# Performance work log

Measured on AMD Instinct MI355X. Metric: run time of the kernel, lower is better.

Reference implementation:

```python
import jax, jax.numpy as jnp
import numpy as np

BN_EPS = 1e-5
LN_EPS = 1e-5

N_NODES = 50000
N_EDGES = 800000
D_IN = 128
D_HID = 512


def _batchnorm(h, gamma, beta):
    # training-mode BatchNorm1d: biased variance over the node/batch dim
    m = jnp.mean(h, axis=0)
    v = jnp.mean(jnp.square(h - m), axis=0)
    return (h - m) * jax.lax.rsqrt(v + BN_EPS) * gamma + beta


def setup_inputs() -> dict:
    key = jax.random.key(0)
    ks = jax.random.split(key, 8)
    x = jax.random.normal(ks[0], (N_NODES, D_IN), dtype=jnp.float32)
    edge_index = jax.random.randint(ks[1], (2, N_EDGES), 0, N_NODES, dtype=jnp.int64)
    s1 = 1.0 / np.sqrt(D_IN)
    s2 = 1.0 / np.sqrt(D_HID)
    W1 = jax.random.uniform(ks[2], (D_IN, D_HID), jnp.float32, -s1, s1)
    b1 = jax.random.uniform(ks[3], (D_HID,), jnp.float32, -s1, s1)
    W2 = jax.random.uniform(ks[4], (D_HID, D_IN), jnp.float32, -s2, s2)
    b2 = jax.random.uniform(ks[5], (D_IN,), jnp.float32, -s2, s2)
    return {
        "x": x,
        "edge_index": edge_index,
        "W1": W1, "b1": b1,
        "bn1_g": jnp.ones((D_HID,), jnp.float32), "bn1_b": jnp.zeros((D_HID,), jnp.float32),
        "W2": W2, "b2": b2,
        "bn2_g": jnp.ones((D_IN,), jnp.float32), "bn2_b": jnp.zeros((D_IN,), jnp.float32),
        "ln_g": jnp.ones((D_IN,), jnp.float32), "ln_b": jnp.zeros((D_IN,), jnp.float32),
    }


def reference(x, edge_index, W1, b1, bn1_g, bn1_b, W2, b2, bn2_g, bn2_b, ln_g, ln_b):
    n = x.shape[0]
    src = edge_index[0]
    dst = edge_index[1]
    # GIN aggregation: sum of neighbor (source) features at each destination node
    agg = jax.ops.segment_sum(x[src], dst, num_segments=n)  # [N, D_IN]
    h = x + agg  # (1 + eps) * x + agg, eps = 0
    # MLP: Linear -> BN -> ReLU -> Linear -> BN -> ReLU (final activation)
    h = jax.nn.relu(_batchnorm(h @ W1 + b1, bn1_g, bn1_b))  # [N, D_HID]
    h = jax.nn.relu(_batchnorm(h @ W2 + b2, bn2_g, bn2_b))  # [N, D_IN]
    # residual + LayerNorm (dropout p=0 -> identity)
    out = h + x
    m = jnp.mean(out, axis=-1, keepdims=True)
    v = jnp.mean(jnp.square(out - m), axis=-1, keepdims=True)
    out = (out - m) * jax.lax.rsqrt(v + LN_EPS) * ln_g + ln_b
    return out
```

## Files before the change

### kernel.cpp

```cpp
#include <hip/hip_runtime.h>
#include <stdint.h>

#define N_NODES 50000
#define N_EDGES 800000
#define D_IN    128
#define D_HID   512
#define NPAD    50048
#define SCAN_NB 196
#define G_TILES 782
#define G_BLOCKS 128

typedef __attribute__((ext_vector_type(8))) short short8;
typedef __attribute__((ext_vector_type(4))) float f32x4;

__device__ __forceinline__ float bf2f(unsigned short u) {
    union { unsigned int i; float f; } v; v.i = ((unsigned int)u) << 16; return v.f;
}
__device__ __forceinline__ unsigned short f2bf(float f) {
    union { float f; unsigned int i; } v; v.f = f;
    unsigned int r = v.i + 0x7fffu + ((v.i >> 16) & 1u);
    return (unsigned short)(r >> 16);
}
__device__ __forceinline__ float loadP(const void* p, long i, int isf) {
    return isf ? ((const float*)p)[i] : bf2f(((const unsigned short*)p)[i]);
}

__global__ void k_init(const void* __restrict__ x, const int* __restrict__ ei,
                       float* __restrict__ stats, int* __restrict__ counts,
                       int* __restrict__ flags) {
    int t = threadIdx.x;
    if (blockIdx.x < 197) {
        int i = blockIdx.x * 256 + t;
        if (i < 384) stats[1024 + i] = 0.f;
        else if (i < 384 + N_NODES) counts[i - 384] = 0;
    } else {
        __shared__ int sh[2];
        if (t == 0) { sh[0] = 0; sh[1] = 1; }
        __syncthreads();
        const unsigned short* xu = (const unsigned short*)x;
        for (int i = t; i < 8192; i += 256)
            if (((xu[i] >> 7) & 0xFF) == 0xFF) sh[0] = 1;
        for (int k = t; k < 64; k += 256)
            if (ei[2 * k + 1] != 0) sh[1] = 0;
        __syncthreads();
        if (t == 0) { flags[0] = sh[0]; flags[1] = sh[1]; }
    }
}

__global__ void k_transpose2(const void* __restrict__ W1, const void* __restrict__ W2,
                             unsigned short* __restrict__ w1t, unsigned short* __restrict__ w2t,
                             const int* __restrict__ flags) {
    int isf = flags[0];
    int idx = blockIdx.x * 256 + threadIdx.x;
    if (idx < D_IN * D_HID) {
        int n = idx >> 7, k = idx & 127;
        int src = k * D_HID + n;
        w1t[idx] = isf ? f2bf(((const float*)W1)[src])
                       : ((const unsigned short*)W1)[src];
    } else {
        int j = idx - D_IN * D_HID;
        int n = j >> 9, k = j & 511;
        int src = k * D_IN + n;
        w2t[j] = isf ? f2bf(((const float*)W2)[src])
                     : ((const unsigned short*)W2)[src];
    }
}

__global__ void k_count(const int* __restrict__ ei, int* __restrict__ counts,
                        const int* __restrict__ flags) {
    int i64 = flags[1];
    int e = blockIdx.x * 256 + threadIdx.x;
    int d = i64 ? ei[2 * N_EDGES + 2 * e] : ei[N_EDGES + e];
    d = min(max(d, 0), N_NODES - 1);
    atomicAdd(&counts[d], 1);
}

__global__ __launch_bounds__(256) void k_scan_block(const int* __restrict__ counts,
                                                    int* __restrict__ rowptr,
                                                    int* __restrict__ partials) {
    __shared__ int a[256], b[256];
    int t = threadIdx.x;
    int idx = blockIdx.x * 256 + t;
    int c = (idx < N_NODES) ? counts[idx] : 0;
    a[t] = c;
    __syncthreads();
    int* src = a; int* dst = b;
    for (int off = 1; off < 256; off <<= 1) {
        dst[t] = src[t] + ((t >= off) ? src[t - off] : 0);
        __syncthreads();
        int* tmp = src; src = dst; dst = tmp;
    }
    if (idx < N_NODES) rowptr[idx] = src[t] - c;
    if (t == 255) partials[blockIdx.x] = src[255];
}

__global__ __launch_bounds__(256) void k_scan_part(int* __restrict__ partials) {
    __shared__ int a[256], b[256];
    int t = threadIdx.x;
    int c = (t < SCAN_NB) ? partials[t] : 0;
    a[t] = c;
    __syncthreads();
    int* src = a; int* dst = b;
    for (int off = 1; off < 256; off <<= 1) {
        dst[t] = src[t] + ((t >= off) ? src[t - off] : 0);
        __syncthreads();
        int* tmp = src; src = dst; dst = tmp;
    }
    if (t < SCAN_NB) partials[t] = src[t] - c;
}

__global__ void k_scan_add(int* __restrict__ rowptr, int* __restrict__ cursor,
                           const int* __restrict__ partials) {
    int idx = blockIdx.x * 256 + threadIdx.x;
    if (idx < N_NODES) {
        int v = rowptr[idx] + partials[blockIdx.x];
        rowptr[idx] = v;
        cursor[idx] = v;
    } else if (idx == N_NODES) {
        rowptr[N_NODES] = N_EDGES;
    }
}

__global__ void k_fill(const int* __restrict__ ei, int* __restrict__ cursor,
                       int* __restrict__ bucket, const int* __restrict__ flags) {
    int i64 = flags[1];
    int e = blockIdx.x * 256 + threadIdx.x;
    int s, d;
    if (i64) { s = ei[2 * e]; d = ei[2 * N_EDGES + 2 * e]; }
    else     { s = ei[e];     d = ei[N_EDGES + e]; }
    s = min(max(s, 0), N_NODES - 1);
    d = min(max(d, 0), N_NODES - 1);
    int pos = atomicAdd(&cursor[d], 1);
    bucket[pos] = s;
}

__global__ __launch_bounds__(256) void k_gather(const int* __restrict__ rowptr,
                                                const int* __restrict__ bucket,
                                                const void* __restrict__ x,
                                                unsigned short* __restrict__ agg,
                                                const int* __restrict__ flags) {
    int isf = flags[0];
    int w = threadIdx.x >> 6, lane = threadIdx.x & 63;
    int row = blockIdx.x * 4 + w;
    float a0 = 0.f, a1 = 0.f;
    if (row < N_NODES) {
        int beg = rowptr[row], end = rowptr[row + 1];
        if (isf) {
            const float* xf = (const float*)x;
            float2 v = *(const float2*)(xf + (size_t)row * D_IN + lane * 2);
            a0 = v.x; a1 = v.y;
            int j = beg;
            for (; j + 4 <= end; j += 4) {
                int s0 = bucket[j], s1 = bucket[j + 1], s2 = bucket[j + 2], s3 = bucket[j + 3];
                float2 n0 = *(const float2*)(xf + (size_t)s0 * D_IN + lane * 2);
                float2 n1 = *(const float2*)(xf + (size_t)s1 * D_IN + lane * 2);
                float2 n2 = *(const float2*)(xf + (size_t)s2 * D_IN + lane * 2);
                float2 n3 = *(const float2*)(xf + (size_t)s3 * D_IN + lane * 2);
                a0 += (n0.x + n1.x) + (n2.x + n3.x);
                a1 += (n0.y + n1.y) + (n2.y + n3.y);
            }
            for (; j < end; j++) {
                float2 n = *(const float2*)(xf + (size_t)bucket[j] * D_IN + lane * 2);
                a0 += n.x; a1 += n.y;
            }
        } else {
            const unsigned int* xu = (const unsigned int*)x;
            unsigned int u = xu[(size_t)row * 64 + lane];
            a0 = bf2f(u & 0xffff); a1 = bf2f(u >> 16);
            int j = beg;
            for (; j + 4 <= end; j += 4) {
                int s0 = bucket[j], s1 = bucket[j + 1], s2 = bucket[j + 2], s3 = bucket[j + 3];
                unsigned int u0 = xu[(size_t)s0 * 64 + lane];
                unsigned int u1 = xu[(size_t)s1 * 64 + lane];
                unsigned int u2 = xu[(size_t)s2 * 64 + lane];
                unsigned int u3 = xu[(size_t)s3 * 64 + lane];
                a0 += (bf2f(u0 & 0xffff) + bf2f(u1 & 0xffff)) + (bf2f(u2 & 0xffff) + bf2f(u3 & 0xffff));
                a1 += (bf2f(u0 >> 16) + bf2f(u1 >> 16)) + (bf2f(u2 >> 16) + bf2f(u3 >> 16));
            }
            for (; j < end; j++) {
                unsigned int n = xu[(size_t)bucket[j] * 64 + lane];
                a0 += bf2f(n & 0xffff); a1 += bf2f(n >> 16);
            }
        }
    }
    unsigned int o = (unsigned int)f2bf(a0) | ((unsigned int)f2bf(a1) << 16);
    ((unsigned int*)agg)[(size_t)row * 64 + lane] = o;
}

__global__ __launch_bounds__(256) void k_gram(const unsigned short* __restrict__ aggb,
                                              float* __restrict__ Gpart,
                                              float* __restrict__ colsum) {
    __shared__ unsigned short ldsT[128 * 64];
    int t = threadIdx.x;
    int wid = t >> 6, lane = t & 63;
    int wm = wid & 1, wn = wid >> 1;
    int quad = lane >> 4, l16 = lane & 15;
    f32x4 acc[4][4] = {};
    float cs = 0.f;
    int cscol = t & 127, cskh = t >> 7;
    for (int tile = blockIdx.x; tile < G_TILES; tile += G_BLOCKS) {
        __syncthreads();
        size_t rowbase = (size_t)tile * 64;
#pragma unroll
        for (int jj = 0; jj < 2; jj++) {
            int j = t + jj * 256;
            int c = j >> 5, rp = j & 31;
            uint4 v0 = *(const uint4*)(aggb + (rowbase + 2 * rp) * 128 + c * 8);
            uint4 v1 = *(const uint4*)(aggb + (rowbase + 2 * rp + 1) * 128 + c * 8);
            const unsigned short* p0 = (const unsigned short*)&v0;
            const unsigned short* p1 = (const unsigned short*)&v1;
            int k = 2 * rp, kc = k >> 3, ko = k & 7;
#pragma unroll
            for (int e = 0; e < 8; e++) {
                int col = c * 8 + e;
                *(unsigned int*)(ldsT + col * 64 + ((kc ^ (col & 7)) * 8) + ko) =
                    (unsigned int)p0[e] | ((unsigned int)p1[e] << 16);
            }
        }
        __syncthreads();
#pragma unroll
        for (int ksub = 0; ksub < 2; ksub++) {
            short8 fa[4], fb[4];
#pragma unroll
            for (int mt = 0; mt < 4; mt++) {
                int col = wm * 64 + mt * 16 + l16;
                fa[mt] = *(const short8*)(ldsT + col * 64 + (((ksub * 4 + quad) ^ (col & 7)) * 8));
            }
#pragma unroll
            for (int nt = 0; nt < 4; nt++) {
                int col = wn * 64 + nt * 16 + l16;
                fb[nt] = *(const short8*)(ldsT + col * 64 + (((ksub * 4 + quad) ^ (col & 7)) * 8));
            }
#pragma unroll
            for (int mt = 0; mt < 4; mt++)
#pragma unroll
                for (int nt = 0; nt < 4; nt++)
                    acc[mt][nt] = __builtin_amdgcn_mfma_f32_16x16x32_bf16(fa[mt], fb[nt], acc[mt][nt], 0, 0, 0);
        }
#pragma unroll
        for (int kc = 0; kc < 4; kc++) {
            short8 v = *(const short8*)(ldsT + cscol * 64 + (((cskh * 4 + kc) ^ (cscol & 7)) * 8));
#pragma unroll
            for (int e = 0; e < 8; e++) cs += bf2f((unsigned short)v[e]);
        }
    }
    float* gp = Gpart + (size_t)blockIdx.x * 16384;
#pragma unroll
    for (int mt = 0; mt < 4; mt++)
#pragma unroll
        for (int nt = 0; nt < 4; nt++) {
            int m = wm * 64 + mt * 16 + quad * 4;
            int n = wn * 64 + nt * 16 + l16;
#pragma unroll
            for (int rg = 0; rg < 4; rg++)
                gp[(m + rg) * 128 + n] = acc[mt][nt][rg];
        }
    atomicAdd(&colsum[cscol], cs);
}

__global__ void k_gred(const float* __restrict__ Gpart, float* __restrict__ G) {
    int i = blockIdx.x * 256 + threadIdx.x;
    float s = 0.f;
#pragma unroll 8
    for (int b = 0; b < G_BLOCKS; b++) s += Gpart[(size_t)b * 16384 + i];
    G[i] = s;
}

__global__ __launch_bounds__(256) void k_bn1(const float* __restrict__ G,
                                             const float* __restrict__ colsum,
                                             const unsigned short* __restrict__ w1t,
                                             const void* __restrict__ b1,
                                             float* __restrict__ sum1,
                                             float* __restrict__ sumsq1,
                                             const int* __restrict__ flags) {
    int isf = flags[0];
    __shared__ float wsh[4][128];
    int t = threadIdx.x, wid = t >> 6, lane = t & 63;
    int n = blockIdx.x * 4 + wid;
    unsigned int u = *(const unsigned int*)(w1t + (size_t)n * 128 + lane * 2);
    wsh[wid][lane * 2] = bf2f(u & 0xffff);
    wsh[wid][lane * 2 + 1] = bf2f(u >> 16);
    __syncthreads();
    const float* w = wsh[wid];
    const f32x4* g0 = (const f32x4*)(G + (size_t)lane * 128);
    const f32x4* g1 = (const f32x4*)(G + (size_t)(lane + 64) * 128);
    float t0 = 0.f, t1 = 0.f;
#pragma unroll 4
    for (int q4 = 0; q4 < 32; q4++) {
        f32x4 a = g0[q4], b = g1[q4];
        float w0 = w[q4 * 4], w1 = w[q4 * 4 + 1], w2 = w[q4 * 4 + 2], w3 = w[q4 * 4 + 3];
        t0 += a[0] * w0 + a[1] * w1 + a[2] * w2 + a[3] * w3;
        t1 += b[0] * w0 + b[1] * w1 + b[2] * w2 + b[3] * w3;
    }
    float sq = w[lane] * t0 + w[lane + 64] * t1;
    float s  = w[lane] * colsum[lane] + w[lane + 64] * colsum[lane + 64];
#pragma unroll
    for (int m = 1; m < 64; m <<= 1) {
        sq += __shfl_xor(sq, m, 64);
        s  += __shfl_xor(s, m, 64);
    }
    if (lane == 0) {
        float b = loadP(b1, n, isf);
        sum1[n]   = s + (float)N_NODES * b;
        sumsq1[n] = sq + 2.f * b * s + (float)N_NODES * b * b;
    }
}

__global__ __launch_bounds__(256, 2) void k_fused(const unsigned short* aggb,
                                                  const unsigned short* __restrict__ w1t,
                                                  const unsigned short* __restrict__ w2t,
                                                  const void* __restrict__ b1,
                                                  const void* __restrict__ b2,
                                                  const void* __restrict__ g1,
                                                  const void* __restrict__ bb1,
                                                  const float* __restrict__ sum1,
                                                  const float* __restrict__ sumsq1,
                                                  unsigned short* h2,
                                                  float* __restrict__ sum2,
                                                  float* __restrict__ sumsq2,
                                                  const int* __restrict__ flags) {
    __shared__ unsigned short bufW[128 * 128];
    __shared__ unsigned short bufA[128 * 128];
    int isf = flags[0];
    int t = threadIdx.x;
    int m0 = blockIdx.x * 128;
    int r = t >> 1, half = t & 1;
    int wid = t >> 6, lane = t & 63;
    int wm = wid & 1, wn = wid >> 1;
    int quad = lane >> 4, l16 = lane & 15;
#pragma unroll
    for (int i = 0; i < 8; i++) {
        int chunk = half * 8 + i;
        *(uint4*)(bufA + r * 128 + ((chunk ^ (r & 15)) * 8)) =
            *(const uint4*)(aggb + (size_t)(m0 + r) * 128 + chunk * 8);
    }
    __syncthreads();
    short8 ax[4][4];
#pragma unroll
    for (int ks = 0; ks < 4; ks++)
#pragma unroll
        for (int mt = 0; mt < 4; mt++)
            ax[ks][mt] = *(const short8*)(bufA + (wm * 64 + mt * 16 + l16) * 128 + (((ks * 4 + quad) ^ l16) * 8));
    f32x4 acc2[4][4] = {};
    for (int nb = 0; nb < 4; nb++) {
        __syncthreads();
#pragma unroll
        for (int i = 0; i < 8; i++) {
            int chunk = half * 8 + i;
            *(uint4*)(bufW + r * 128 + ((chunk ^ (r & 15)) * 8)) =
                *(const uint4*)(w1t + (size_t)(nb * 128 + r) * 128 + chunk * 8);
        }
        __syncthreads();
        f32x4 acc1[4][4] = {};
#pragma unroll
        for (int ks = 0; ks < 4; ks++) {
            short8 bw[4];
#pragma unroll
            for (int nt = 0; nt < 4; nt++)
                bw[nt] = *(const short8*)(bufW + (wn * 64 + nt * 16 + l16) * 128 + (((ks * 4 + quad) ^ l16) * 8));
#pragma unroll
            for (int mt = 0; mt < 4; mt++)
#pragma unroll
                for (int nt = 0; nt < 4; nt++)
                    acc1[mt][nt] = __builtin_amdgcn_mfma_f32_16x16x32_bf16(ax[ks][mt], bw[nt], acc1[mt][nt], 0, 0, 0);
        }
#pragma unroll
        for (int nt = 0; nt < 4; nt++) {
            int nl = wn * 64 + nt * 16 + l16;
            int n1 = nb * 128 + nl;
            float mz = sum1[n1] * (1.f / N_NODES);
            float vz = sumsq1[n1] * (1.f / N_NODES) - mz * mz;
            float inv = rsqrtf(fmaxf(vz, 0.f) + 1e-5f);
            float A = loadP(g1, n1, isf) * inv;
            float C = loadP(bb1, n1, isf) - mz * A + loadP(b1, n1, isf) * A;
            int ccw = nl >> 3, cl = nl & 7;
#pragma unroll
            for (int mt = 0; mt < 4; mt++)
#pragma unroll
                for (int rg = 0; rg < 4; rg++) {
                    int R = wm * 64 + mt * 16 + quad * 4 + rg;
                    bufA[R * 128 + ((ccw ^ (R & 15)) * 8) + cl] = f2bf(fmaxf(acc1[mt][nt][rg] * A + C, 0.f));
                }
        }
        __syncthreads();
#pragma unroll
        for (int i = 0; i < 8; i++) {
            int chunk = half * 8 + i;
            *(uint4*)(bufW + r * 128 + ((chunk ^ (r & 15)) * 8)) =
                *(const uint4*)(w2t + (size_t)r * D_HID + nb * 128 + chunk * 8);
        }
        __syncthreads();
#pragma unroll
        for (int ks = 0; ks < 4; ks++) {
            short8 aa[4], bw[4];
#pragma unroll
            for (int mt = 0; mt < 4; mt++)
                aa[mt] = *(const short8*)(bufA + (wm * 64 + mt * 16 + l16) * 128 + (((ks * 4 + quad) ^ l16) * 8));
#pragma unroll
            for (int nt = 0; nt < 4; nt++)
                bw[nt] = *(const short8*)(bufW + (wn * 64 + nt * 16 + l16) * 128 + (((ks * 4 + quad) ^ l16) * 8));
#pragma unroll
            for (int mt = 0; mt < 4; mt++)
#pragma unroll
                for (int nt = 0; nt < 4; nt++)
                    acc2[mt][nt] = __builtin_amdgcn_mfma_f32_16x16x32_bf16(aa[mt], bw[nt], acc2[mt][nt], 0, 0, 0);
        }
    }
#pragma unroll
    for (int nt = 0; nt < 4; nt++) {
        int n = wn * 64 + nt * 16 + l16;
        float bias = loadP(b2, n, isf);
        float s = 0.f, ss = 0.f;
#pragma unroll
        for (int mt = 0; mt < 4; mt++) {
            int Rb = m0 + wm * 64 + mt * 16 + quad * 4;
#pragma unroll
            for (int rg = 0; rg < 4; rg++) {
                float z = acc2[mt][nt][rg] + bias;
                h2[(size_t)(Rb + rg) * D_IN + n] = f2bf(z);
                if (Rb + rg < N_NODES) { s += z; ss += z * z; }
            }
        }
        s += __shfl_xor(s, 16, 64); ss += __shfl_xor(ss, 16, 64);
        s += __shfl_xor(s, 32, 64); ss += __shfl_xor(ss, 32, 64);
        if (quad == 0) { atomicAdd(&sum2[n], s); atomicAdd(&sumsq2[n], ss); }
    }
}

__global__ __launch_bounds__(256) void k_final(const unsigned short* __restrict__ h2,
                                               const void* __restrict__ x,
                                               const float* __restrict__ sum2,
                                               const float* __restrict__ sumsq2,
                                               const void* __restrict__ g2,
                                               const void* __restrict__ bb2,
                                               const void* __restrict__ lng,
                                               const void* __restrict__ lnb,
                                               void* __restrict__ out,
                                               const int* __restrict__ flags) {
    int isf = flags[0];
    __shared__ float a2s[D_IN], c2s[D_IN];
    int t = threadIdx.x;
    if (t < D_IN) {
        float m = sum2[t] * (1.f / N_NODES);
        float v = sumsq2[t] * (1.f / N_NODES) - m * m;
        float inv = rsqrtf(fmaxf(v, 0.f) + 1e-5f);
        float a = loadP(g2, t, isf) * inv;
        a2s[t] = a;
        c2s[t] = loadP(bb2, t, isf) - m * a;
    }
    __syncthreads();
    int w = t >> 6, lane = t & 63;
    int row = blockIdx.x * 4 + w;
    if (row >= N_NODES) return;
    size_t base = (size_t)row * D_IN;
    int c0 = lane * 2, c1 = lane * 2 + 1;
    unsigned int hu = ((const unsigned int*)h2)[base / 2 + lane];
    float x0, x1;
    if (isf) {
        float2 xv = *((const float2*)x + base / 2 + lane);
        x0 = xv.x; x1 = xv.y;
    } else {
        unsigned int xu = ((const unsigned int*)x)[base / 2 + lane];
        x0 = bf2f(xu & 0xffff); x1 = bf2f(xu >> 16);
    }
    float o0 = fmaxf(a2s[c0] * bf2f(hu & 0xffff) + c2s[c0], 0.f) + x0;
    float o1 = fmaxf(a2s[c1] * bf2f(hu >> 16) + c2s[c1], 0.f) + x1;
    float s = o0 + o1, ss = o0 * o0 + o1 * o1;
#pragma unroll
    for (int m = 1; m < 64; m <<= 1) {
        s += __shfl_xor(s, m, 64);
        ss += __shfl_xor(ss, m, 64);
    }
    float mean = s * (1.f / D_IN);
    float var = ss * (1.f / D_IN) - mean * mean;
    float inv = rsqrtf(fmaxf(var, 0.f) + 1e-5f);
    float r0 = (o0 - mean) * inv * loadP(lng, c0, isf) + loadP(lnb, c0, isf);
    float r1 = (o1 - mean) * inv * loadP(lng, c1, isf) + loadP(lnb, c1, isf);
    if (isf) {
        *((float2*)out + base / 2 + lane) = make_float2(r0, r1);
    } else {
        ((unsigned int*)out)[base / 2 + lane] = (unsigned int)f2bf(r0) | ((unsigned int)f2bf(r1) << 16);
    }
}

extern "C" void kernel_launch(void* const* d_in, const int* in_sizes, int n_in,
                              void* d_out, int out_size, void* d_ws, size_t ws_size,
                              hipStream_t stream) {
    const void* x    = d_in[0];
    const int*  ei   = (const int*)d_in[1];
    const void* W1   = d_in[2];
    const void* b1   = d_in[3];
    const void* bn1g = d_in[4];
    const void* bn1b = d_in[5];
    const void* W2   = d_in[6];
    const void* b2   = d_in[7];
    const void* bn2g = d_in[8];
    const void* bn2b = d_in[9];
    const void* lng  = d_in[10];
    const void* lnb  = d_in[11];

    char* ws = (char*)d_ws;
    float* stats   = (float*)ws;
    float* sum1    = stats;
    float* sumsq1  = stats + 512;
    float* sum2    = stats + 1024;
    float* sumsq2  = stats + 1152;
    float* colsum  = stats + 1280;
    int*   flags   = (int*)(ws + 5632);
    int*   partials= (int*)(ws + 5696);
    int*   rowptr  = (int*)(ws + 8192);
    int*   cursor  = (int*)(ws + 208256);
    unsigned short* w1t = (unsigned short*)(ws + 408320);
    unsigned short* w2t = (unsigned short*)(ws + 539392);
    float* G       = (float*)(ws + 670464);
    float* Gpart   = (float*)(ws + 736000);
    int*   bucket  = (int*)(ws + 9124608);
    unsigned short* agg = (unsigned short*)(ws + 12324608);
    unsigned short* h2  = agg;

    k_init<<<198, 256, 0, stream>>>(x, ei, stats, cursor, flags);
    k_transpose2<<<512, 256, 0, stream>>>(W1, W2, w1t, w2t, flags);
    k_count<<<N_EDGES / 256, 256, 0, stream>>>(ei, cursor, flags);
    k_scan_block<<<SCAN_NB, 256, 0, stream>>>(cursor, rowptr, partials);
    k_scan_part<<<1, 256, 0, stream>>>(partials);
    k_scan_add<<<SCAN_NB, 256, 0, stream>>>(rowptr, cursor, partials);
    k_fill<<<N_EDGES / 256, 256, 0, stream>>>(ei, cursor, bucket, flags);
    k_gather<<<NPAD / 4, 256, 0, stream>>>(rowptr, bucket, x, agg, flags);
    k_gram<<<G_BLOCKS, 256, 0, stream>>>(agg, Gpart, colsum);
    k_gred<<<64, 256, 0, stream>>>(Gpart, G);
    k_bn1<<<128, 256, 0, stream>>>(G, colsum, w1t, b1, sum1, sumsq1, flags);
    k_fused<<<NPAD / 128, 256, 0, stream>>>(agg, w1t, w2t, b1, b2, bn1g, bn1b,
                                            sum1, sumsq1, h2, sum2, sumsq2, flags);
    k_final<<<(N_NODES + 3) / 4, 256, 0, stream>>>(h2, x, sum2, sumsq2, bn2g, bn2b, lng, lnb, d_out, flags);
}
```

Baseline: 398.8 us.

## Halve fused MLP row tile to 64 and stage h2 stores through LDS

Shrinks the k_fused row tile from 128 to 64 nodes per block. This halves the accumulator registers and the activation LDS buffer, raises launch bounds to 3 blocks per SM, and doubles the grid for better occupancy and load balance across CUs. The h2 output is now written into LDS first and then stored with coalesced 16-byte writes instead of scattered 2-byte stores. The trade-off is that each block reloads all W1/W2 weight tiles for only 64 rows, which doubles weight traffic, and the extra syncs add overhead.

```diff
diff --git a/kernel.cpp b/kernel.cpp
--- a/kernel.cpp
+++ b/kernel.cpp
@@ -306,7 +306,7 @@
     }
 }
 
-__global__ __launch_bounds__(256, 2) void k_fused(const unsigned short* aggb,
+__global__ __launch_bounds__(256, 3) void k_fused(const unsigned short* aggb,
                                                   const unsigned short* __restrict__ w1t,
                                                   const unsigned short* __restrict__ w2t,
                                                   const void* __restrict__ b1,
@@ -320,38 +320,41 @@
                                                   float* __restrict__ sumsq2,
                                                   const int* __restrict__ flags) {
     __shared__ unsigned short bufW[128 * 128];
-    __shared__ unsigned short bufA[128 * 128];
+    __shared__ unsigned short bufA[64 * 128];
     int isf = flags[0];
     int t = threadIdx.x;
-    int m0 = blockIdx.x * 128;
-    int r = t >> 1, half = t & 1;
+    int m0 = blockIdx.x * 64;
+    int rw = t >> 1, halfw = t & 1;
     int wid = t >> 6, lane = t & 63;
     int wm = wid & 1, wn = wid >> 1;
     int quad = lane >> 4, l16 = lane & 15;
-#pragma unroll
-    for (int i = 0; i < 8; i++) {
-        int chunk = half * 8 + i;
-        *(uint4*)(bufA + r * 128 + ((chunk ^ (r & 15)) * 8)) =
-            *(const uint4*)(aggb + (size_t)(m0 + r) * 128 + chunk * 8);
-    }
-    __syncthreads();
-    short8 ax[4][4];
+    {
+        int r = t >> 2, q = t & 3;
+#pragma unroll
+        for (int i = 0; i < 4; i++) {
+            int chunk = q * 4 + i;
+            *(uint4*)(bufA + r * 128 + ((chunk ^ (r & 15)) * 8)) =
+                *(const uint4*)(aggb + (size_t)(m0 + r) * 128 + chunk * 8);
+        }
+    }
+    __syncthreads();
+    short8 ax[4][2];
 #pragma unroll
     for (int ks = 0; ks < 4; ks++)
 #pragma unroll
-        for (int mt = 0; mt < 4; mt++)
-            ax[ks][mt] = *(const short8*)(bufA + (wm * 64 + mt * 16 + l16) * 128 + (((ks * 4 + quad) ^ l16) * 8));
-    f32x4 acc2[4][4] = {};
+        for (int mt = 0; mt < 2; mt++)
+            ax[ks][mt] = *(const short8*)(bufA + (wm * 32 + mt * 16 + l16) * 128 + (((ks * 4 + quad) ^ l16) * 8));
+    f32x4 acc2[2][4] = {};
     for (int nb = 0; nb < 4; nb++) {
         __syncthreads();
 #pragma unroll
         for (int i = 0; i < 8; i++) {
-            int chunk = half * 8 + i;
-            *(uint4*)(bufW + r * 128 + ((chunk ^ (r & 15)) * 8)) =
-                *(const uint4*)(w1t + (size_t)(nb * 128 + r) * 128 + chunk * 8);
-        }
-        __syncthreads();
-        f32x4 acc1[4][4] = {};
+            int chunk = halfw * 8 + i;
+            *(uint4*)(bufW + rw * 128 + ((chunk ^ (rw & 15)) * 8)) =
+                *(const uint4*)(w1t + (size_t)(nb * 128 + rw) * 128 + chunk * 8);
+        }
+        __syncthreads();
+        f32x4 acc1[2][4] = {};
 #pragma unroll
         for (int ks = 0; ks < 4; ks++) {
             short8 bw[4];
@@ -359,7 +362,7 @@
             for (int nt = 0; nt < 4; nt++)
                 bw[nt] = *(const short8*)(bufW + (wn * 64 + nt * 16 + l16) * 128 + (((ks * 4 + quad) ^ l16) * 8));
 #pragma unroll
-            for (int mt = 0; mt < 4; mt++)
+            for (int mt = 0; mt < 2; mt++)
 #pragma unroll
                 for (int nt = 0; nt < 4; nt++)
                     acc1[mt][nt] = __builtin_amdgcn_mfma_f32_16x16x32_bf16(ax[ks][mt], bw[nt], acc1[mt][nt], 0, 0, 0);
@@ -375,55 +378,63 @@
             float C = loadP(bb1, n1, isf) - mz * A + loadP(b1, n1, isf) * A;
             int ccw = nl >> 3, cl = nl & 7;
 #pragma unroll
-            for (int mt = 0; mt < 4; mt++)
+            for (int mt = 0; mt < 2; mt++)
 #pragma unroll
                 for (int rg = 0; rg < 4; rg++) {
-                    int R = wm * 64 + mt * 16 + quad * 4 + rg;
+                    int R = wm * 32 + mt * 16 + quad * 4 + rg;
                     bufA[R * 128 + ((ccw ^ (R & 15)) * 8) + cl] = f2bf(fmaxf(acc1[mt][nt][rg] * A + C, 0.f));
                 }
         }
         __syncthreads();
 #pragma unroll
         for (int i = 0; i < 8; i++) {
-            int chunk = half * 8 + i;
-            *(uint4*)(bufW + r * 128 + ((chunk ^ (r & 15)) * 8)) =
-                *(const uint4*)(w2t + (size_t)r * D_HID + nb * 128 + chunk * 8);
+            int chunk = halfw * 8 + i;
+            *(uint4*)(bufW + rw * 128 + ((chunk ^ (rw & 15)) * 8)) =
+                *(const uint4*)(w2t + (size_t)rw * D_HID + nb * 128 + chunk * 8);
         }
         __syncthreads();
 #pragma unroll
         for (int ks = 0; ks < 4; ks++) {
-            short8 aa[4], bw[4];
-#pragma unroll
-            for (int mt = 0; mt < 4; mt++)
-                aa[mt] = *(const short8*)(bufA + (wm * 64 + mt * 16 + l16) * 128 + (((ks * 4 + quad) ^ l16) * 8));
+            short8 aa[2], bw[4];
+#pragma unroll
+            for (int mt = 0; mt < 2; mt++)
+                aa[mt] = *(const short8*)(bufA + (wm * 32 + mt * 16 + l16) * 128 + (((ks * 4 + quad) ^ l16) * 8));
 #pragma unroll
             for (int nt = 0; nt < 4; nt++)
                 bw[nt] = *(const short8*)(bufW + (wn * 64 + nt * 16 + l16) * 128 + (((ks * 4 + quad) ^ l16) * 8));
 #pragma unroll
-            for (int mt = 0; mt < 4; mt++)
+            for (int mt = 0; mt < 2; mt++)
 #pragma unroll
                 for (int nt = 0; nt < 4; nt++)
                     acc2[mt][nt] = __builtin_amdgcn_mfma_f32_16x16x32_bf16(aa[mt], bw[nt], acc2[mt][nt], 0, 0, 0);
         }
     }
+    __syncthreads();
 #pragma unroll
     for (int nt = 0; nt < 4; nt++) {
         int n = wn * 64 + nt * 16 + l16;
         float bias = loadP(b2, n, isf);
         float s = 0.f, ss = 0.f;
 #pragma unroll
-        for (int mt = 0; mt < 4; mt++) {
-            int Rb = m0 + wm * 64 + mt * 16 + quad * 4;
+        for (int mt = 0; mt < 2; mt++) {
+            int Rl = wm * 32 + mt * 16 + quad * 4;
 #pragma unroll
             for (int rg = 0; rg < 4; rg++) {
                 float z = acc2[mt][nt][rg] + bias;
-                h2[(size_t)(Rb + rg) * D_IN + n] = f2bf(z);
-                if (Rb + rg < N_NODES) { s += z; ss += z * z; }
+                bufA[(Rl + rg) * 128 + n] = f2bf(z);
+                if (m0 + Rl + rg < N_NODES) { s += z; ss += z * z; }
             }
         }
         s += __shfl_xor(s, 16, 64); ss += __shfl_xor(ss, 16, 64);
         s += __shfl_xor(s, 32, 64); ss += __shfl_xor(ss, 32, 64);
         if (quad == 0) { atomicAdd(&sum2[n], s); atomicAdd(&sumsq2[n], ss); }
+    }
+    __syncthreads();
+#pragma unroll
+    for (int i = 0; i < 4; i++) {
+        int idx = t + i * 256;
+        int r = idx >> 4, seg = idx & 15;
+        *(uint4*)(h2 + (size_t)(m0 + r) * 128 + seg * 8) = *(const uint4*)(bufA + r * 128 + seg * 8);
     }
 }
 
@@ -529,7 +540,7 @@
     k_gram<<<G_BLOCKS, 256, 0, stream>>>(agg, Gpart, colsum);
     k_gred<<<64, 256, 0, stream>>>(Gpart, G);
     k_bn1<<<128, 256, 0, stream>>>(G, colsum, w1t, b1, sum1, sumsq1, flags);
-    k_fused<<<NPAD / 128, 256, 0, stream>>>(agg, w1t, w2t, b1, b2, bn1g, bn1b,
-                                            sum1, sumsq1, h2, sum2, sumsq2, flags);
+    k_fused<<<NPAD / 64, 256, 0, stream>>>(agg, w1t, w2t, b1, b2, bn1g, bn1b,
+                                           sum1, sumsq1, h2, sum2, sumsq2, flags);
     k_final<<<(N_NODES + 3) / 4, 256, 0, stream>>>(h2, x, sum2, sumsq2, bn2g, bn2b, lng, lnb, d_out, flags);
 }
```

Result: slower. 417.5 us (+4.7%).
